# Performance work log

Hardware: AMD Instinct MI355X
Metric: run time of the kernel (lower is better)

## Reference

```python
import jax, jax.numpy as jnp
import numpy as np


def _layernorm(x, g, b, eps=1e-5):
    m = x.mean(-1, keepdims=True)
    v = ((x - m) ** 2).mean(-1, keepdims=True)
    return (x - m) / jnp.sqrt(v + eps) * g + b


def _rotate_every_two(x):
    x1 = x[..., ::2]
    x2 = x[..., 1::2]
    return jnp.stack([-x2, x1], axis=-1).reshape(x.shape)


def _segsum(x):
    # x: (..., L) of negative decay rates -> (..., L, L) bidirectional segment sums
    cs = jnp.cumsum(x, axis=-1)
    d = cs[..., :, None] - cs[..., None, :]
    L = x.shape[-1]
    i = jnp.arange(L)[:, None]
    j = jnp.arange(L)[None, :]
    # lower-tri (incl diag): cs[i]-cs[j]; strict upper: cs[j]-cs[i]; diag is 0
    return jnp.where(i >= j, d, -d)


def _forward(x, y, th, dw1_w, dw1_b, dw2_w, dw2_b, qw, qb, kw, kb, vw, vb,
             lepe_w, lepe_b, dt_w, dt_bias, A_log, ow, ob,
             n1_g, n1_b, ffn_w1, ffn_b1, ffn_w2, ffn_b2, n2_g, n2_b):
    B, C, H, W = x.shape
    nh = dt_bias.shape[0]
    hd = C // nh
    scaling = hd ** (-0.5)

    # dynamic gated fusion of the two kv branches (1x1 convs == channel matmuls)
    fusion = jnp.concatenate([y, th], axis=1)                      # (B,2C,H,W)
    hid = jax.nn.relu(jnp.einsum('bchw,oc->bohw', fusion, dw1_w) + dw1_b[None, :, None, None])
    logits = jnp.einsum('bchw,oc->bohw', hid, dw2_w) + dw2_b[None, :, None, None]
    wts = jax.nn.softmax(logits, axis=1)                           # (B,2,H,W)
    fused = y * wts[:, 0:1] + th * wts[:, 1:2]

    xh = jnp.transpose(x, (0, 2, 3, 1))                            # (B,H,W,C)
    fkv = jnp.transpose(fused, (0, 2, 3, 1))

    # 2D RoPE tables (flattened raster index)
    angle = jnp.repeat(1.0 / 10000 ** jnp.linspace(0.0, 1.0, hd // 2), 2)
    idx = jnp.arange(H * W, dtype=x.dtype)
    sin = jnp.sin(idx[:, None] * angle[None, :]).reshape(H, W, hd)
    cos = jnp.cos(idx[:, None] * angle[None, :]).reshape(H, W, hd)

    q = xh @ qw + qb
    k = fkv @ kw + kb
    v = fkv @ vw + vb

    # depthwise 5x5 conv position term on v (NHWC)
    lepe = jax.lax.conv_general_dilated(
        v, lepe_w, (1, 1), ((2, 2), (2, 2)),
        dimension_numbers=('NHWC', 'HWIO', 'NHWC'), feature_group_count=C) + lepe_b

    k = k * scaling
    q = q.reshape(B, H, W, nh, hd).transpose(0, 3, 1, 2, 4)        # (B,nh,H,W,hd)
    k = k.reshape(B, H, W, nh, hd).transpose(0, 3, 1, 2, 4)
    v5 = v.reshape(B, H, W, nh, hd).transpose(0, 3, 1, 2, 4)

    qr = q * cos + _rotate_every_two(q) * sin
    kr = k * cos + _rotate_every_two(k) * sin

    # PathEmbeding2D: data-dependent decay masks
    xt = xh.reshape(B, H * W, nh, hd)
    dt = xt @ dt_w                                                 # (B,S,nh,2)
    A = -jnp.exp(A_log)                                            # (nh,)
    da = jax.nn.softplus(dt[..., 0] + dt_bias) * A                 # (B,S,nh)
    db = jax.nn.softplus(dt[..., 1] + dt_bias) * A
    mask_w = _segsum(da.reshape(B, H, W, nh).transpose(0, 1, 3, 2))  # (B,H,nh,W,W)
    mask_h = _segsum(db.reshape(B, H, W, nh).transpose(0, 2, 3, 1))  # (B,W,nh,H,H)

    # row (width-direction) and column (height-direction) attentions
    qk_w = jax.nn.softmax(jnp.einsum('bnhid,bnhjd->bhnij', qr, kr) + mask_w, axis=-1)  # (B,H,nh,W,W)
    qk_h = jax.nn.softmax(jnp.einsum('bnhwd,bngwd->bwnhg', qr, kr) + mask_h, axis=-1)  # (B,W,nh,H,H)

    v_w = jnp.einsum('bhnij,bnhjd->bhnid', qk_w, v5)               # (B,H,nh,W,hd)
    out1 = jnp.einsum('bwnhg,bgnwd->bwnhd', qk_h, v_w)             # (B,W,nh,H,hd)
    out1 = out1.transpose(0, 3, 1, 2, 4).reshape(B, H, W, C)

    v_h = jnp.einsum('bwnhg,bngwd->bwnhd', qk_h, v5)               # (B,W,nh,H,hd)
    out2 = jnp.einsum('bhnij,bjnhd->bhnid', qk_w, v_h)             # (B,H,nh,W,hd)
    out2 = out2.transpose(0, 1, 3, 2, 4).reshape(B, H, W, C)

    out = 0.5 * out1 + 0.5 * out2 + lepe
    out = out @ ow + ob
    out = _layernorm(xh + out, n1_g, n1_b)
    ffn = jax.nn.gelu(out @ ffn_w1 + ffn_b1, approximate=False) @ ffn_w2 + ffn_b2
    out = _layernorm(out + ffn, n2_g, n2_b)
    return jnp.transpose(out, (0, 3, 1, 2))                        # (B,C,H,W)


def setup_inputs() -> dict:
    B, C, H, W, nh = 4, 64, 128, 128, 4
    hd = C // nh
    key = jax.random.key(0)
    ks = jax.random.split(key, 20)
    n = lambda k, shp, s: jax.random.normal(k, shp, dtype=jnp.float32) * s
    rng = np.random.default_rng(0)
    dt = np.exp(rng.uniform(0.0, 1.0, nh) * (np.log(0.1) - np.log(0.001)) + np.log(0.001))
    dt = np.clip(dt, 1e-4, None)
    dt_bias = jnp.asarray(dt + np.log(-np.expm1(-dt)), dtype=jnp.float32)
    A_log = jnp.asarray(np.log(rng.uniform(1.0, 1.1, nh)), dtype=jnp.float32)
    inp = {
        'x': n(ks[0], (B, C, H, W), 1.0),
        'y': n(ks[1], (B, C, H, W), 1.0),
        'th': n(ks[2], (B, C, H, W), 1.0),
        'dw1_w': n(ks[3], (C, 2 * C), (2 * C) ** -0.5),
        'dw1_b': jnp.zeros((C,), jnp.float32),
        'dw2_w': n(ks[4], (2, C), C ** -0.5),
        'dw2_b': jnp.zeros((2,), jnp.float32),
        'qw': n(ks[5], (C, C), 0.2 * C ** -0.5),
        'qb': jnp.zeros((C,), jnp.float32),
        'kw': n(ks[6], (C, C), 0.2 * C ** -0.5),
        'kb': jnp.zeros((C,), jnp.float32),
        'vw': n(ks[7], (C, C), 0.2 * C ** -0.5),
        'vb': jnp.zeros((C,), jnp.float32),
        'lepe_w': n(ks[8], (5, 5, 1, C), 0.1),
        'lepe_b': jnp.zeros((C,), jnp.float32),
        'dt_w': n(ks[9], (hd, 2), hd ** -0.5),
        'dt_bias': dt_bias,
        'A_log': A_log,
        'ow': n(ks[10], (C, C), C ** -0.5),
        'ob': jnp.zeros((C,), jnp.float32),
        'n1_g': jnp.ones((C,), jnp.float32),
        'n1_b': jnp.zeros((C,), jnp.float32),
        'ffn_w1': n(ks[11], (C, 4 * C), C ** -0.5),
        'ffn_b1': jnp.zeros((4 * C,), jnp.float32),
        'ffn_w2': n(ks[12], (4 * C, C), (4 * C) ** -0.5),
        'ffn_b2': jnp.zeros((C,), jnp.float32),
        'n2_g': jnp.ones((C,), jnp.float32),
        'n2_b': jnp.zeros((C,), jnp.float32),
    }
    return inp


def reference(x, y, th, dw1_w, dw1_b, dw2_w, dw2_b, qw, qb, kw, kb, vw, vb,
              lepe_w, lepe_b, dt_w, dt_bias, A_log, ow, ob,
              n1_g, n1_b, ffn_w1, ffn_b1, ffn_w2, ffn_b2, n2_g, n2_b):
    return _forward(x, y, th, dw1_w, dw1_b, dw2_w, dw2_b, qw, qb, kw, kb, vw, vb,
                    lepe_w, lepe_b, dt_w, dt_bias, A_log, ow, ob,
                    n1_g, n1_b, ffn_w1, ffn_b1, ffn_w2, ffn_b2, n2_g, n2_b)
```

## Files before the change

### kernel.cpp

```cpp
#include <hip/hip_runtime.h>
#include <math.h>

#define HWSZ 16384

typedef __attribute__((ext_vector_type(8))) short bf16x8;
typedef __attribute__((ext_vector_type(4))) float f32x4;
typedef unsigned short u16;

union U4 { uint4 v; u16 s[8]; };
union U2 { uint2 v; u16 s[4]; };

__device__ __forceinline__ float gelu_f(float v) {
    return 0.5f * v * (1.0f + erff(v * 0.70710678118654752f));
}
__device__ __forceinline__ float splus_f(float v) {
    return (v > 20.f) ? v : log1pf(expf(v));
}
__device__ __forceinline__ u16 f2bf(float f) {
    union { float f; unsigned u; } v; v.f = f;
    unsigned r = (v.u + 0x7FFF + ((v.u >> 16) & 1)) >> 16;
    return (u16)r;
}
__device__ __forceinline__ unsigned pk2(float a, float b) {
    return (unsigned)f2bf(a) | ((unsigned)f2bf(b) << 16);
}
__device__ __forceinline__ float bf2f(u16 s) {
    union { unsigned u; float f; } v; v.u = ((unsigned)s) << 16; return v.f;
}

__global__ __launch_bounds__(256) void k_prep(
    const float* __restrict__ w1, const float* __restrict__ qw,
    const float* __restrict__ kw, const float* __restrict__ vw,
    const float* __restrict__ ow, const float* __restrict__ fw1s,
    const float* __restrict__ fw2s, u16* __restrict__ wout)
{
    int id = blockIdx.x*256 + threadIdx.x;
    float v;
    if (id < 8192) {
        v = w1[id];
    } else if (id < 20480) {
        int t = id - 8192; int m = t >> 12;
        int i = t & 4095; int o = i >> 6, c = i & 63;
        const float* src = (m==0) ? qw : ((m==1) ? kw : vw);
        v = src[c*64 + o];
        if (m == 1) v *= 0.25f;
    } else if (id < 24576) {
        int i = id - 20480; int c = i >> 6, k = i & 63;
        v = ow[k*64 + c];
    } else if (id < 40960) {
        int i = id - 24576; int o = i >> 6, k = i & 63;
        v = fw1s[k*256 + o];
    } else {
        int i = id - 40960; int jc = i >> 12; int r = i & 4095;
        int c = r >> 6, k2 = r & 63;
        v = fw2s[(jc*64 + k2)*64 + c];
    }
    wout[id] = f2bf(v);
}

#define FS 136
__global__ __launch_bounds__(256) void k_fuse(
    const float* __restrict__ y, const float* __restrict__ th,
    const u16* __restrict__ wfuse, const float* __restrict__ b1,
    const float* __restrict__ w2, const float* __restrict__ b2,
    u16* __restrict__ fused)
{
    __shared__ u16 Fsh[128*FS];
    __shared__ u16 Wt[64*FS];
    int tid = threadIdx.x, bid = blockIdx.x;
    int pbase = bid*128;
    int b = pbase >> 14, p0 = pbase & 16383;
    for (int vi = tid; vi < 1024; vi += 256) {
        int cp = vi >> 5;
        int p4 = (vi & 31)*4;
        int c0 = cp*2;
        float4 a = *(const float4*)&y [((size_t)(b*64+c0  ))*HWSZ + p0 + p4];
        float4 c = *(const float4*)&y [((size_t)(b*64+c0+1))*HWSZ + p0 + p4];
        *(unsigned*)&Fsh[(p4+0)*FS + c0] = pk2(a.x, c.x);
        *(unsigned*)&Fsh[(p4+1)*FS + c0] = pk2(a.y, c.y);
        *(unsigned*)&Fsh[(p4+2)*FS + c0] = pk2(a.z, c.z);
        *(unsigned*)&Fsh[(p4+3)*FS + c0] = pk2(a.w, c.w);
        float4 e = *(const float4*)&th[((size_t)(b*64+c0  ))*HWSZ + p0 + p4];
        float4 f = *(const float4*)&th[((size_t)(b*64+c0+1))*HWSZ + p0 + p4];
        *(unsigned*)&Fsh[(p4+0)*FS + 64 + c0] = pk2(e.x, f.x);
        *(unsigned*)&Fsh[(p4+1)*FS + 64 + c0] = pk2(e.y, f.y);
        *(unsigned*)&Fsh[(p4+2)*FS + 64 + c0] = pk2(e.z, f.z);
        *(unsigned*)&Fsh[(p4+3)*FS + 64 + c0] = pk2(e.w, f.w);
    }
    for (int vi = tid; vi < 1024; vi += 256) {
        int o = vi >> 4, s8 = (vi & 15)*8;
        *(uint4*)&Wt[o*FS + s8] = *(const uint4*)&wfuse[o*128 + s8];
    }
    __syncthreads();
    int lane = tid & 63, wv = tid >> 6;
    int quad = lane >> 4, lm = lane & 15;
    int M0 = wv*32;
    f32x4 z = {0.f,0.f,0.f,0.f};
    f32x4 acc[2][4];
    #pragma unroll
    for (int mt = 0; mt < 2; ++mt)
        #pragma unroll
        for (int nt = 0; nt < 4; ++nt) acc[mt][nt] = z;
    #pragma unroll
    for (int ks = 0; ks < 4; ++ks) {
        bf16x8 aF[2];
        #pragma unroll
        for (int mt = 0; mt < 2; ++mt)
            aF[mt] = *(bf16x8*)&Fsh[(M0+mt*16+lm)*FS + ks*32 + quad*8];
        #pragma unroll
        for (int nt = 0; nt < 4; ++nt) {
            bf16x8 bW = *(bf16x8*)&Wt[(nt*16+lm)*FS + ks*32 + quad*8];
            #pragma unroll
            for (int mt = 0; mt < 2; ++mt)
                acc[mt][nt] = __builtin_amdgcn_mfma_f32_16x16x32_bf16(aF[mt], bW, acc[mt][nt], 0,0,0);
        }
    }
    float b1v[4], w2av[4], w2bv[4];
    #pragma unroll
    for (int nt = 0; nt < 4; ++nt) {
        int o = nt*16 + lm;
        b1v[nt] = b1[o]; w2av[nt] = w2[o]; w2bv[nt] = w2[64+o];
    }
    float bias2a = b2[0], bias2b = b2[1];
    size_t gbase = (size_t)(b*16384 + p0);
    #pragma unroll
    for (int mt = 0; mt < 2; ++mt) {
        #pragma unroll
        for (int r = 0; r < 4; ++r) {
            int p = M0 + mt*16 + quad*4 + r;
            float l0 = 0.f, l1 = 0.f;
            #pragma unroll
            for (int nt = 0; nt < 4; ++nt) {
                float h = fmaxf(acc[mt][nt][r] + b1v[nt], 0.f);
                l0 += h * w2av[nt];
                l1 += h * w2bv[nt];
            }
            l0 += __shfl_xor(l0,1,64); l0 += __shfl_xor(l0,2,64);
            l0 += __shfl_xor(l0,4,64); l0 += __shfl_xor(l0,8,64);
            l1 += __shfl_xor(l1,1,64); l1 += __shfl_xor(l1,2,64);
            l1 += __shfl_xor(l1,4,64); l1 += __shfl_xor(l1,8,64);
            l0 += bias2a; l1 += bias2b;
            float m = fmaxf(l0, l1);
            float e0 = __expf(l0 - m), e1 = __expf(l1 - m);
            float inv = 1.f/(e0 + e1);
            float wa = e0*inv, wb = e1*inv;
            U2 yv, tv;
            yv.v = *(uint2*)&Fsh[p*FS + lm*4];
            tv.v = *(uint2*)&Fsh[p*FS + 64 + lm*4];
            unsigned o0 = pk2(bf2f(yv.s[0])*wa + bf2f(tv.s[0])*wb,
                              bf2f(yv.s[1])*wa + bf2f(tv.s[1])*wb);
            unsigned o1 = pk2(bf2f(yv.s[2])*wa + bf2f(tv.s[2])*wb,
                              bf2f(yv.s[3])*wa + bf2f(tv.s[3])*wb);
            *(uint2*)&fused[(gbase + p)*64 + lm*4] = make_uint2(o0, o1);
        }
    }
}

__global__ __launch_bounds__(256) void k_qkv(
    const float* __restrict__ x, const u16* __restrict__ fused,
    const u16* __restrict__ bq, const float* __restrict__ qb,
    const u16* __restrict__ bk, const float* __restrict__ kb,
    const u16* __restrict__ bv, const float* __restrict__ vb,
    const float* __restrict__ dtw, const float* __restrict__ dtb,
    const float* __restrict__ alog,
    u16* __restrict__ qr, u16* __restrict__ kr, u16* __restrict__ v5,
    float* __restrict__ da, float* __restrict__ db)
{
    __shared__ u16 Ax[128*72];
    __shared__ u16 Af[128*72];
    __shared__ u16 Bq[64*72], Bk[64*72], Bv[64*72];
    int tid = threadIdx.x, bid = blockIdx.x;
    int pbase = bid*128;
    int b = pbase >> 14, p0 = pbase & 16383;
    for (int vi = tid; vi < 1024; vi += 256) {
        int cp = vi >> 5, p4 = (vi & 31)*4;
        int c0 = cp*2;
        float4 a = *(const float4*)&x[((size_t)(b*64+c0  ))*HWSZ + p0 + p4];
        float4 c = *(const float4*)&x[((size_t)(b*64+c0+1))*HWSZ + p0 + p4];
        *(unsigned*)&Ax[(p4+0)*72 + c0] = pk2(a.x, c.x);
        *(unsigned*)&Ax[(p4+1)*72 + c0] = pk2(a.y, c.y);
        *(unsigned*)&Ax[(p4+2)*72 + c0] = pk2(a.z, c.z);
        *(unsigned*)&Ax[(p4+3)*72 + c0] = pk2(a.w, c.w);
    }
    for (int vi = tid; vi < 1024; vi += 256) {
        int p = vi >> 3, seg = (vi & 7)*8;
        *(uint4*)&Af[p*72 + seg] = *(const uint4*)&fused[((size_t)(b*16384) + p0 + p)*64 + seg];
    }
    for (int vi = tid; vi < 1536; vi += 256) {
        int m = vi >> 9;
        int i = vi & 511;
        int o = i >> 3, s8 = (i & 7)*8;
        const u16* src = (m==0) ? bq : ((m==1) ? bk : bv);
        u16* dst = (m==0) ? Bq : ((m==1) ? Bk : Bv);
        *(uint4*)&dst[o*72 + s8] = *(const uint4*)&src[o*64 + s8];
    }
    __syncthreads();
    int lane = tid & 63, wv = tid >> 6;
    int quad = lane >> 4, lm = lane & 15;
    int M0 = wv*32;
    f32x4 z = {0.f,0.f,0.f,0.f};
    f32x4 accQ[2][4], accK[2][4], accV[2][4];
    #pragma unroll
    for (int mt = 0; mt < 2; ++mt)
        #pragma unroll
        for (int nt = 0; nt < 4; ++nt) { accQ[mt][nt]=z; accK[mt][nt]=z; accV[mt][nt]=z; }
    #pragma unroll
    for (int ks = 0; ks < 2; ++ks) {
        bf16x8 aX[2], aF[2];
        #pragma unroll
        for (int mt = 0; mt < 2; ++mt) {
            aX[mt] = *(bf16x8*)&Ax[(M0+mt*16+lm)*72 + ks*32 + quad*8];
            aF[mt] = *(bf16x8*)&Af[(M0+mt*16+lm)*72 + ks*32 + quad*8];
        }
        #pragma unroll
        for (int nt = 0; nt < 4; ++nt) {
            bf16x8 bQ = *(bf16x8*)&Bq[(nt*16+lm)*72 + ks*32 + quad*8];
            bf16x8 bK = *(bf16x8*)&Bk[(nt*16+lm)*72 + ks*32 + quad*8];
            bf16x8 bV = *(bf16x8*)&Bv[(nt*16+lm)*72 + ks*32 + quad*8];
            #pragma unroll
            for (int mt = 0; mt < 2; ++mt) {
                accQ[mt][nt] = __builtin_amdgcn_mfma_f32_16x16x32_bf16(aX[mt], bQ, accQ[mt][nt], 0,0,0);
                accK[mt][nt] = __builtin_amdgcn_mfma_f32_16x16x32_bf16(aF[mt], bK, accK[mt][nt], 0,0,0);
                accV[mt][nt] = __builtin_amdgcn_mfma_f32_16x16x32_bf16(aF[mt], bV, accV[mt][nt], 0,0,0);
            }
        }
    }
    {
        float dtw_[32];
        #pragma unroll
        for (int i = 0; i < 32; ++i) dtw_[i] = dtw[i];
        #pragma unroll
        for (int rep = 0; rep < 2; ++rep) {
            int pair = tid + rep*256;
            int p = pair >> 2, n = pair & 3;
            float dt0 = 0.f, dt1 = 0.f;
            #pragma unroll
            for (int d = 0; d < 16; ++d) {
                float xv = bf2f(Ax[p*72 + n*16 + d]);
                dt0 += xv*dtw_[2*d];
                dt1 += xv*dtw_[2*d+1];
            }
            float A = -expf(alog[n]);
            float bb = dtb[n];
            int P = p0 + p;
            int h = P >> 7, w = P & 127;
            da[((b*128+h)*4+n)*128 + w] = splus_f(dt0+bb)*A;
            db[((b*128+w)*4+n)*128 + h] = splus_f(dt1+bb)*A;
        }
    }
    float qbv[4], kbv[4], vbv[4];
    #pragma unroll
    for (int nt = 0; nt < 4; ++nt) {
        qbv[nt] = qb[nt*16+lm]; kbv[nt] = kb[nt*16+lm]*0.25f; vbv[nt] = vb[nt*16+lm];
    }
    bool evn = !(lm & 1);
    float ang = exp2f(-1.89824462565f * (float)(lm >> 1));
    int bb4 = b*4;
    #pragma unroll
    for (int mt = 0; mt < 2; ++mt) {
        #pragma unroll
        for (int r = 0; r < 4; ++r) {
            int P = p0 + M0 + mt*16 + quad*4 + r;
            float sn_, cs_;
            sincosf((float)P * ang, &sn_, &cs_);
            #pragma unroll
            for (int nt = 0; nt < 4; ++nt) {
                float vq = accQ[mt][nt][r] + qbv[nt];
                float pq = __shfl_xor(vq, 1, 64);
                float rq = evn ? vq*cs_ - pq*sn_ : vq*cs_ + pq*sn_;
                unsigned uq = f2bf(rq);
                unsigned upq = (unsigned)__shfl_xor((int)uq, 1, 64);
                float vk = accK[mt][nt][r] + kbv[nt];
                float pk = __shfl_xor(vk, 1, 64);
                float rk = evn ? vk*cs_ - pk*sn_ : vk*cs_ + pk*sn_;
                unsigned uk = f2bf(rk);
                unsigned upk = (unsigned)__shfl_xor((int)uk, 1, 64);
                unsigned uv = f2bf(accV[mt][nt][r] + vbv[nt]);
                unsigned upv = (unsigned)__shfl_xor((int)uv, 1, 64);
                if (evn) {
                    size_t off = ((size_t)(bb4+nt)*HWSZ + P)*16 + lm;
                    *(unsigned*)&qr[off] = (uq & 0xffff) | (upq << 16);
                    *(unsigned*)&kr[off] = (uk & 0xffff) | (upk << 16);
                    *(unsigned*)&v5[off] = (uv & 0xffff) | (upv << 16);
                }
            }
        }
    }
}

#define LROW 328
__global__ __launch_bounds__(256) void k_lepe(
    const u16* __restrict__ v5, const float* __restrict__ lw,
    const float* __restrict__ lb, u16* __restrict__ lepe)
{
    __shared__ float sv[36*LROW];
    __shared__ float swt[400];
    int tid = threadIdx.x, bid = blockIdx.x;
    int tw = bid & 7, th_ = (bid >> 3) & 3, n = (bid >> 5) & 3, b = bid >> 7;
    int bn = b*4 + n;
    int h0 = th_*32, w0 = tw*16;
    for (int i = tid; i < 400; i += 256) {
        int tap = i >> 4, d = i & 15;
        swt[i] = lw[tap*64 + n*16 + d];
    }
    const u16* vb = v5 + (size_t)bn*HWSZ*16;
    for (int vi = tid; vi < 1440; vi += 256) {
        int cell = vi >> 1, half = vi & 1;
        int hh = cell/20, ww = cell - hh*20;
        int h = h0 - 2 + hh, w = w0 - 2 + ww;
        U4 val; val.v = make_uint4(0,0,0,0);
        if (h >= 0 && h < 128 && w >= 0 && w < 128)
            val.v = *(const uint4*)&vb[((size_t)(h*128+w))*16 + half*8];
        float* dst = &sv[hh*LROW + ww*16 + half*8];
        #pragma unroll
        for (int u = 0; u < 8; ++u) dst[u] = bf2f(val.s[u]);
    }
    __syncthreads();
    int df = (tid & 3)*4;
    int s  = tid >> 2;
    int ph = s >> 1;
    int pw = (s & 1)*8;
    float4 bv = *(const float4*)&lb[n*16 + df];
    float acc[8][4];
    #pragma unroll
    for (int ow = 0; ow < 8; ++ow) {
        acc[ow][0] = bv.x; acc[ow][1] = bv.y; acc[ow][2] = bv.z; acc[ow][3] = bv.w;
    }
    #pragma unroll
    for (int ky = 0; ky < 5; ++ky) {
        float wgt[5][4];
        #pragma unroll
        for (int kx = 0; kx < 5; ++kx) {
            float4 wv = *(const float4*)&swt[(ky*5+kx)*16 + df];
            wgt[kx][0]=wv.x; wgt[kx][1]=wv.y; wgt[kx][2]=wv.z; wgt[kx][3]=wv.w;
        }
        float dat[13][4];
        #pragma unroll
        for (int c = 0; c < 13; ++c) {
            float4 dv = *(const float4*)&sv[(ph+ky)*LROW + (pw+c)*16 + df];
            dat[c][0]=dv.x; dat[c][1]=dv.y; dat[c][2]=dv.z; dat[c][3]=dv.w;
        }
        #pragma unroll
        for (int ow = 0; ow < 8; ++ow)
            #pragma unroll
            for (int kx = 0; kx < 5; ++kx)
                #pragma unroll
                for (int u = 0; u < 4; ++u)
                    acc[ow][u] += dat[ow+kx][u]*wgt[kx][u];
    }
    u16* ob = lepe + ((size_t)bn*HWSZ + (size_t)(h0+ph)*128 + w0+pw)*16 + df;
    #pragma unroll
    for (int ow = 0; ow < 8; ++ow)
        *(uint2*)&ob[ow*16] = make_uint2(pk2(acc[ow][0],acc[ow][1]), pk2(acc[ow][2],acc[ow][3]));
}

__global__ __launch_bounds__(256) void k_attn_w1(
    const u16* __restrict__ qr, const u16* __restrict__ kr,
    const u16* __restrict__ v5, const float* __restrict__ dacs,
    u16* __restrict__ vwb)
{
    __shared__ u16 Vt[16*136], Ps[128*136];
    __shared__ float csr[128];
    int tid = threadIdx.x, bid = blockIdx.x;
    int h = bid & 127, n = (bid >> 7) & 3, b = bid >> 9;
    size_t rowoff = ((size_t)((b*4+n)*128 + h)) * 2048;
    {
        int jp = tid >> 2, q4 = tid & 3;
        U2 a, c;
        a.v = *(const uint2*)&v5[rowoff + (2*jp)*16 + q4*4];
        c.v = *(const uint2*)&v5[rowoff + (2*jp+1)*16 + q4*4];
        #pragma unroll
        for (int u = 0; u < 4; ++u)
            *(unsigned*)&Vt[(q4*4+u)*136 + 2*jp] = (unsigned)a.s[u] | ((unsigned)c.s[u] << 16);
    }
    if (tid < 128) csr[tid] = dacs[((b*128+h)*4+n)*128 + tid];
    __syncthreads();
    if (tid < 64) {
        float2 e = *(float2*)&csr[tid*2];
        float s = e.x + e.y;
        #pragma unroll
        for (int d = 1; d < 64; d <<= 1) {
            float t = __shfl_up(s, d, 64);
            if (tid >= d) s += t;
        }
        csr[tid*2]   = s - e.y;
        csr[tid*2+1] = s;
    }
    __syncthreads();
    int lane = tid & 63, wv = tid >> 6;
    int quad = lane >> 4, lm = lane & 15;
    int r0 = wv*32, r1 = wv*32 + 16;
    bf16x8 z8 = {0,0,0,0,0,0,0,0};
    bf16x8 aQ0 = z8, aQ1 = z8;
    if (quad < 2) {
        aQ0 = *(const bf16x8*)&qr[rowoff + (size_t)(r0+lm)*16 + quad*8];
        aQ1 = *(const bf16x8*)&qr[rowoff + (size_t)(r1+lm)*16 + quad*8];
    }
    float csj[8], csi0[4], csi1[4];
    #pragma unroll
    for (int jt = 0; jt < 8; ++jt) csj[jt] = csr[jt*16+lm];
    #pragma unroll
    for (int r = 0; r < 4; ++r) { csi0[r] = csr[r0+quad*4+r]; csi1[r] = csr[r1+quad*4+r]; }
    float ls0[4]={0,0,0,0}, ls1[4]={0,0,0,0};
    f32x4 z = {0.f,0.f,0.f,0.f};
    #pragma unroll
    for (int jt = 0; jt < 8; ++jt) {
        bf16x8 bK = z8;
        if (quad < 2) bK = *(const bf16x8*)&kr[rowoff + (size_t)(jt*16+lm)*16 + quad*8];
        f32x4 s0 = __builtin_amdgcn_mfma_f32_16x16x32_bf16(aQ0, bK, z, 0,0,0);
        f32x4 s1 = __builtin_amdgcn_mfma_f32_16x16x32_bf16(aQ1, bK, z, 0,0,0);
        #pragma unroll
        for (int r = 0; r < 4; ++r) {
            float e0 = __expf(s0[r] - fabsf(csi0[r]-csj[jt])); ls0[r] += e0;
            float e1 = __expf(s1[r] - fabsf(csi1[r]-csj[jt])); ls1[r] += e1;
            Ps[(r0+quad*4+r)*136 + jt*16+lm] = f2bf(e0);
            Ps[(r1+quad*4+r)*136 + jt*16+lm] = f2bf(e1);
        }
    }
    float inv0[4], inv1[4];
    #pragma unroll
    for (int r = 0; r < 4; ++r) {
        #pragma unroll
        for (int m = 1; m < 16; m <<= 1) {
            ls0[r] += __shfl_xor(ls0[r], m, 64);
            ls1[r] += __shfl_xor(ls1[r], m, 64);
        }
        inv0[r] = 1.f/ls0[r]; inv1[r] = 1.f/ls1[r];
    }
    __syncthreads();
    f32x4 acc0 = z, acc1 = z;
    #pragma unroll
    for (int c = 0; c < 4; ++c) {
        bf16x8 bV  = *(bf16x8*)&Vt[lm*136 + c*32 + quad*8];
        bf16x8 aP0 = *(bf16x8*)&Ps[(r0+lm)*136 + c*32 + quad*8];
        bf16x8 aP1 = *(bf16x8*)&Ps[(r1+lm)*136 + c*32 + quad*8];
        acc0 = __builtin_amdgcn_mfma_f32_16x16x32_bf16(aP0, bV, acc0, 0,0,0);
        acc1 = __builtin_amdgcn_mfma_f32_16x16x32_bf16(aP1, bV, acc1, 0,0,0);
    }
    bool evn = !(lm & 1);
    #pragma unroll
    for (int r = 0; r < 4; ++r) {
        int i0 = r0+quad*4+r, i1 = r1+quad*4+r;
        unsigned u0 = f2bf(acc0[r]*inv0[r]);
        unsigned u1 = f2bf(acc1[r]*inv1[r]);
        unsigned up0 = (unsigned)__shfl_xor((int)u0, 1, 64);
        unsigned up1 = (unsigned)__shfl_xor((int)u1, 1, 64);
        if (evn) {
            *(unsigned*)&vwb[rowoff + (size_t)i0*16 + lm] = (u0 & 0xffff) | (up0 << 16);
            *(unsigned*)&vwb[rowoff + (size_t)i1*16 + lm] = (u1 & 0xffff) | (up1 << 16);
        }
    }
}

__global__ __launch_bounds__(256) void k_attn_h(
    const u16* __restrict__ qr, const u16* __restrict__ kr,
    const u16* __restrict__ v5, const u16* __restrict__ vwb,
    const float* __restrict__ dbcs,
    u16* __restrict__ vhb, u16* __restrict__ o1b)
{
    __shared__ u16 Vt[16*136], Wt[16*136], Ps[128*136];
    __shared__ float csr[128];
    int tid = threadIdx.x, bid = blockIdx.x;
    int w = bid & 127, n = (bid >> 7) & 3, b = bid >> 9;
    int bn = b*4 + n;
    size_t base = ((size_t)bn*16384 + w)*16;
    {
        int jp = tid >> 2, q4 = tid & 3;
        U2 a, c, e, f;
        a.v = *(const uint2*)&v5 [base + (size_t)(2*jp)*2048 + q4*4];
        c.v = *(const uint2*)&v5 [base + (size_t)(2*jp+1)*2048 + q4*4];
        e.v = *(const uint2*)&vwb[base + (size_t)(2*jp)*2048 + q4*4];
        f.v = *(const uint2*)&vwb[base + (size_t)(2*jp+1)*2048 + q4*4];
        #pragma unroll
        for (int u = 0; u < 4; ++u) {
            *(unsigned*)&Vt[(q4*4+u)*136 + 2*jp] = (unsigned)a.s[u] | ((unsigned)c.s[u] << 16);
            *(unsigned*)&Wt[(q4*4+u)*136 + 2*jp] = (unsigned)e.s[u] | ((unsigned)f.s[u] << 16);
        }
    }
    if (tid < 128) csr[tid] = dbcs[((b*128+w)*4+n)*128 + tid];
    __syncthreads();
    if (tid < 64) {
        float2 e = *(float2*)&csr[tid*2];
        float s = e.x + e.y;
        #pragma unroll
        for (int d = 1; d < 64; d <<= 1) {
            float t = __shfl_up(s, d, 64);
            if (tid >= d) s += t;
        }
        csr[tid*2]   = s - e.y;
        csr[tid*2+1] = s;
    }
    __syncthreads();
    int lane = tid & 63, wv = tid >> 6;
    int quad = lane >> 4, lm = lane & 15;
    int r0 = wv*32, r1 = wv*32 + 16;
    bf16x8 z8 = {0,0,0,0,0,0,0,0};
    bf16x8 aQ0 = z8, aQ1 = z8;
    if (quad < 2) {
        aQ0 = *(const bf16x8*)&qr[base + (size_t)(r0+lm)*2048 + quad*8];
        aQ1 = *(const bf16x8*)&qr[base + (size_t)(r1+lm)*2048 + quad*8];
    }
    float csj[8], csi0[4], csi1[4];
    #pragma unroll
    for (int jt = 0; jt < 8; ++jt) csj[jt] = csr[jt*16+lm];
    #pragma unroll
    for (int r = 0; r < 4; ++r) { csi0[r] = csr[r0+quad*4+r]; csi1[r] = csr[r1+quad*4+r]; }
    float ls0[4]={0,0,0,0}, ls1[4]={0,0,0,0};
    f32x4 z = {0.f,0.f,0.f,0.f};
    #pragma unroll
    for (int jt = 0; jt < 8; ++jt) {
        bf16x8 bK = z8;
        if (quad < 2) bK = *(const bf16x8*)&kr[base + (size_t)(jt*16+lm)*2048 + quad*8];
        f32x4 s0 = __builtin_amdgcn_mfma_f32_16x16x32_bf16(aQ0, bK, z, 0,0,0);
        f32x4 s1 = __builtin_amdgcn_mfma_f32_16x16x32_bf16(aQ1, bK, z, 0,0,0);
        #pragma unroll
        for (int r = 0; r < 4; ++r) {
            float e0 = __expf(s0[r] - fabsf(csi0[r]-csj[jt])); ls0[r] += e0;
            float e1 = __expf(s1[r] - fabsf(csi1[r]-csj[jt])); ls1[r] += e1;
            Ps[(r0+quad*4+r)*136 + jt*16+lm] = f2bf(e0);
            Ps[(r1+quad*4+r)*136 + jt*16+lm] = f2bf(e1);
        }
    }
    float inv0[4], inv1[4];
    #pragma unroll
    for (int r = 0; r < 4; ++r) {
        #pragma unroll
        for (int m = 1; m < 16; m <<= 1) {
            ls0[r] += __shfl_xor(ls0[r], m, 64);
            ls1[r] += __shfl_xor(ls1[r], m, 64);
        }
        inv0[r] = 1.f/ls0[r]; inv1[r] = 1.f/ls1[r];
    }
    __syncthreads();
    f32x4 aV0 = z, aV1 = z, aW0 = z, aW1 = z;
    #pragma unroll
    for (int c = 0; c < 4; ++c) {
        bf16x8 bV  = *(bf16x8*)&Vt[lm*136 + c*32 + quad*8];
        bf16x8 bW  = *(bf16x8*)&Wt[lm*136 + c*32 + quad*8];
        bf16x8 aP0 = *(bf16x8*)&Ps[(r0+lm)*136 + c*32 + quad*8];
        bf16x8 aP1 = *(bf16x8*)&Ps[(r1+lm)*136 + c*32 + quad*8];
        aV0 = __builtin_amdgcn_mfma_f32_16x16x32_bf16(aP0, bV, aV0, 0,0,0);
        aV1 = __builtin_amdgcn_mfma_f32_16x16x32_bf16(aP1, bV, aV1, 0,0,0);
        aW0 = __builtin_amdgcn_mfma_f32_16x16x32_bf16(aP0, bW, aW0, 0,0,0);
        aW1 = __builtin_amdgcn_mfma_f32_16x16x32_bf16(aP1, bW, aW1, 0,0,0);
    }
    size_t obase = ((size_t)bn*16384 + (size_t)w*128)*16;
    bool evn = !(lm & 1);
    #pragma unroll
    for (int r = 0; r < 4; ++r) {
        int i0 = r0+quad*4+r, i1 = r1+quad*4+r;
        float v0 = inv0[r], v1 = inv1[r];
        unsigned a0 = f2bf(aV0[r]*v0), a1 = f2bf(aV1[r]*v1);
        unsigned b0 = f2bf(aW0[r]*v0), b1 = f2bf(aW1[r]*v1);
        unsigned ap0 = (unsigned)__shfl_xor((int)a0,1,64), ap1 = (unsigned)__shfl_xor((int)a1,1,64);
        unsigned bp0 = (unsigned)__shfl_xor((int)b0,1,64), bp1 = (unsigned)__shfl_xor((int)b1,1,64);
        if (evn) {
            *(unsigned*)&vhb[obase + (size_t)i0*16 + lm] = (a0 & 0xffff) | (ap0 << 16);
            *(unsigned*)&vhb[obase + (size_t)i1*16 + lm] = (a1 & 0xffff) | (ap1 << 16);
            *(unsigned*)&o1b[obase + (size_t)i0*16 + lm] = (b0 & 0xffff) | (bp0 << 16);
            *(unsigned*)&o1b[obase + (size_t)i1*16 + lm] = (b1 & 0xffff) | (bp1 << 16);
        }
    }
}

__global__ __launch_bounds__(256) void k_attn_w2(
    const u16* __restrict__ qr, const u16* __restrict__ kr,
    const u16* __restrict__ vhb, const u16* __restrict__ o1b,
    const float* __restrict__ dacs, const u16* __restrict__ lepe,
    u16* __restrict__ attn)
{
    __shared__ u16 Vt[16*136], Ps[128*136];
    __shared__ float csr[128];
    int tid = threadIdx.x, bid = blockIdx.x;
    int h = bid & 127, n = (bid >> 7) & 3, b = bid >> 9;
    int bn = b*4 + n;
    size_t rowoff = ((size_t)(bn*128 + h)) * 2048;
    size_t vbase  = (size_t)bn*262144 + (size_t)h*16;
    {
        int jp = tid >> 2, q4 = tid & 3;
        U2 a, c;
        a.v = *(const uint2*)&vhb[vbase + (size_t)(2*jp)*2048 + q4*4];
        c.v = *(const uint2*)&vhb[vbase + (size_t)(2*jp+1)*2048 + q4*4];
        #pragma unroll
        for (int u = 0; u < 4; ++u)
            *(unsigned*)&Vt[(q4*4+u)*136 + 2*jp] = (unsigned)a.s[u] | ((unsigned)c.s[u] << 16);
    }
    if (tid < 128) csr[tid] = dacs[((b*128+h)*4+n)*128 + tid];
    __syncthreads();
    if (tid < 64) {
        float2 e = *(float2*)&csr[tid*2];
        float s = e.x + e.y;
        #pragma unroll
        for (int d = 1; d < 64; d <<= 1) {
            float t = __shfl_up(s, d, 64);
            if (tid >= d) s += t;
        }
        csr[tid*2]   = s - e.y;
        csr[tid*2+1] = s;
    }
    __syncthreads();
    int lane = tid & 63, wv = tid >> 6;
    int quad = lane >> 4, lm = lane & 15;
    int r0 = wv*32, r1 = wv*32 + 16;
    bf16x8 z8 = {0,0,0,0,0,0,0,0};
    bf16x8 aQ0 = z8, aQ1 = z8;
    if (quad < 2) {
        aQ0 = *(const bf16x8*)&qr[rowoff + (size_t)(r0+lm)*16 + quad*8];
        aQ1 = *(const bf16x8*)&qr[rowoff + (size_t)(r1+lm)*16 + quad*8];
    }
    float csj[8], csi0[4], csi1[4];
    #pragma unroll
    for (int jt = 0; jt < 8; ++jt) csj[jt] = csr[jt*16+lm];
    #pragma unroll
    for (int r = 0; r < 4; ++r) { csi0[r] = csr[r0+quad*4+r]; csi1[r] = csr[r1+quad*4+r]; }
    float ls0[4]={0,0,0,0}, ls1[4]={0,0,0,0};
    f32x4 z = {0.f,0.f,0.f,0.f};
    #pragma unroll
    for (int jt = 0; jt < 8; ++jt) {
        bf16x8 bK = z8;
        if (quad < 2) bK = *(const bf16x8*)&kr[rowoff + (size_t)(jt*16+lm)*16 + quad*8];
        f32x4 s0 = __builtin_amdgcn_mfma_f32_16x16x32_bf16(aQ0, bK, z, 0,0,0);
        f32x4 s1 = __builtin_amdgcn_mfma_f32_16x16x32_bf16(aQ1, bK, z, 0,0,0);
        #pragma unroll
        for (int r = 0; r < 4; ++r) {
            float e0 = __expf(s0[r] - fabsf(csi0[r]-csj[jt])); ls0[r] += e0;
            float e1 = __expf(s1[r] - fabsf(csi1[r]-csj[jt])); ls1[r] += e1;
            Ps[(r0+quad*4+r)*136 + jt*16+lm] = f2bf(e0);
            Ps[(r1+quad*4+r)*136 + jt*16+lm] = f2bf(e1);
        }
    }
    float inv0[4], inv1[4];
    #pragma unroll
    for (int r = 0; r < 4; ++r) {
        #pragma unroll
        for (int m = 1; m < 16; m <<= 1) {
            ls0[r] += __shfl_xor(ls0[r], m, 64);
            ls1[r] += __shfl_xor(ls1[r], m, 64);
        }
        inv0[r] = 1.f/ls0[r]; inv1[r] = 1.f/ls1[r];
    }
    __syncthreads();
    f32x4 acc0 = z, acc1 = z;
    #pragma unroll
    for (int c = 0; c < 4; ++c) {
        bf16x8 bV  = *(bf16x8*)&Vt[lm*136 + c*32 + quad*8];
        bf16x8 aP0 = *(bf16x8*)&Ps[(r0+lm)*136 + c*32 + quad*8];
        bf16x8 aP1 = *(bf16x8*)&Ps[(r1+lm)*136 + c*32 + quad*8];
        acc0 = __builtin_amdgcn_mfma_f32_16x16x32_bf16(aP0, bV, acc0, 0,0,0);
        acc1 = __builtin_amdgcn_mfma_f32_16x16x32_bf16(aP1, bV, acc1, 0,0,0);
    }
    size_t lpb = (size_t)bn*262144 + (size_t)h*2048;
    size_t oab = (size_t)b*1048576 + (size_t)h*8192 + n*16;
    bool evn = !(lm & 1);
    #pragma unroll
    for (int r = 0; r < 4; ++r) {
        int i0 = r0+quad*4+r, i1 = r1+quad*4+r;
        float o2a = acc0[r]*inv0[r];
        float o2b = acc1[r]*inv1[r];
        float o1a = bf2f(o1b[vbase + (size_t)i0*2048 + lm]);
        float o1c = bf2f(o1b[vbase + (size_t)i1*2048 + lm]);
        float la  = bf2f(lepe[lpb + (size_t)i0*16 + lm]);
        float lc  = bf2f(lepe[lpb + (size_t)i1*16 + lm]);
        unsigned ua = f2bf(0.5f*(o1a + o2a) + la);
        unsigned uc = f2bf(0.5f*(o1c + o2b) + lc);
        unsigned upa = (unsigned)__shfl_xor((int)ua,1,64);
        unsigned upc = (unsigned)__shfl_xor((int)uc,1,64);
        if (evn) {
            *(unsigned*)&attn[oab + (size_t)i0*64 + lm] = (ua & 0xffff) | (upa << 16);
            *(unsigned*)&attn[oab + (size_t)i1*64 + lm] = (uc & 0xffff) | (upc << 16);
        }
    }
}

__global__ __launch_bounds__(256) void k_proj_ln(
    const u16* __restrict__ attn, const float* __restrict__ x,
    const u16* __restrict__ bo, const float* __restrict__ ob,
    const float* __restrict__ g1, const float* __restrict__ b1,
    u16* __restrict__ t1)
{
    __shared__ u16 As[64*72];
    __shared__ u16 Bs[64*72];
    __shared__ float XT[64*68];
    int tid = threadIdx.x, bid = blockIdx.x;
    int pbase = bid*64;
    int b = pbase >> 14, p0 = pbase & 16383;
    for (int vi = tid; vi < 512; vi += 256) {
        int p = vi >> 3, s8 = (vi & 7)*8;
        *(uint4*)&As[p*72 + s8] = *(const uint4*)&attn[((size_t)(pbase+p))*64 + s8];
    }
    for (int vi = tid; vi < 512; vi += 256) {
        int c = vi >> 3, s8 = (vi & 7)*8;
        *(uint4*)&Bs[c*72 + s8] = *(const uint4*)&bo[c*64 + s8];
    }
    for (int vi = tid; vi < 1024; vi += 256) {
        int c = vi >> 4, p4 = (vi & 15)*4;
        *(float4*)&XT[c*68 + p4] = *(const float4*)&x[((size_t)(b*64+c))*HWSZ + p0 + p4];
    }
    __syncthreads();
    int lane = tid & 63, wv = tid >> 6;
    int quad = lane >> 4, lm = lane & 15;
    int M0 = wv*16;
    float xv[4][4], obv[4], g1v[4], b1v[4];
    #pragma unroll
    for (int nt = 0; nt < 4; ++nt) {
        int c = nt*16 + lm;
        obv[nt] = ob[c]; g1v[nt] = g1[c]; b1v[nt] = b1[c];
        #pragma unroll
        for (int r = 0; r < 4; ++r)
            xv[nt][r] = XT[c*68 + M0 + quad*4 + r];
    }
    f32x4 z = {0.f,0.f,0.f,0.f};
    f32x4 acc[4];
    #pragma unroll
    for (int nt = 0; nt < 4; ++nt) acc[nt] = z;
    #pragma unroll
    for (int ks = 0; ks < 2; ++ks) {
        bf16x8 aF = *(bf16x8*)&As[(M0+lm)*72 + ks*32 + quad*8];
        #pragma unroll
        for (int nt = 0; nt < 4; ++nt) {
            bf16x8 bF = *(bf16x8*)&Bs[(nt*16+lm)*72 + ks*32 + quad*8];
            acc[nt] = __builtin_amdgcn_mfma_f32_16x16x32_bf16(aF, bF, acc[nt], 0,0,0);
        }
    }
    float val[4][4], res[4][4];
    #pragma unroll
    for (int r = 0; r < 4; ++r) {
        float s = 0.f;
        #pragma unroll
        for (int nt = 0; nt < 4; ++nt) {
            val[nt][r] = acc[nt][r] + obv[nt] + xv[nt][r];
            s += val[nt][r];
        }
        s += __shfl_xor(s, 1, 64); s += __shfl_xor(s, 2, 64);
        s += __shfl_xor(s, 4, 64); s += __shfl_xor(s, 8, 64);
        float mean = s*(1.f/64.f);
        float vv = 0.f;
        #pragma unroll
        for (int nt = 0; nt < 4; ++nt) {
            float d = val[nt][r] - mean;
            vv += d*d;
        }
// ... 107 lines not shown
        #pragma unroll
        for (int nt = 0; nt < 4; ++nt) {
            float tv = bf2f(At1[pos*72 + nt*16 + lm]);
            val[nt][r] = acc2[nt][r] + sb2v[nt] + tv;
            s += val[nt][r];
        }
        s += __shfl_xor(s, 1, 64); s += __shfl_xor(s, 2, 64);
        s += __shfl_xor(s, 4, 64); s += __shfl_xor(s, 8, 64);
        float mean = s*(1.f/64.f);
        float vv = 0.f;
        #pragma unroll
        for (int nt = 0; nt < 4; ++nt) {
            float d = val[nt][r] - mean;
            vv += d*d;
        }
        vv += __shfl_xor(vv, 1, 64); vv += __shfl_xor(vv, 2, 64);
        vv += __shfl_xor(vv, 4, 64); vv += __shfl_xor(vv, 8, 64);
        float rs = rsqrtf(vv*(1.f/64.f) + 1e-5f);
        #pragma unroll
        for (int nt = 0; nt < 4; ++nt)
            res[nt][r] = (val[nt][r] - mean)*rs*sgv[nt] + sbbv[nt];
    }
    __syncthreads();
    float* outT = (float*)SL;
    #pragma unroll
    for (int r = 0; r < 4; ++r)
        #pragma unroll
        for (int nt = 0; nt < 4; ++nt)
            outT[(nt*16+lm)*68 + M0 + quad*4 + r] = res[nt][r];
    __syncthreads();
    for (int vi = tid; vi < 1024; vi += 256) {
        int c = vi >> 4, p4 = (vi & 15)*4;
        *(float4*)&outp[((size_t)(b*64+c))*HWSZ + p0 + p4] = *(const float4*)&outT[c*68 + p4];
    }
}

extern "C" void kernel_launch(void* const* d_in, const int* in_sizes, int n_in,
                              void* d_out, int out_size, void* d_ws, size_t ws_size,
                              hipStream_t stream) {
    const float* x      = (const float*)d_in[0];
    const float* y      = (const float*)d_in[1];
    const float* th     = (const float*)d_in[2];
    const float* dw1_w  = (const float*)d_in[3];
    const float* dw1_b  = (const float*)d_in[4];
    const float* dw2_w  = (const float*)d_in[5];
    const float* dw2_b  = (const float*)d_in[6];
    const float* qw     = (const float*)d_in[7];
    const float* qb     = (const float*)d_in[8];
    const float* kw     = (const float*)d_in[9];
    const float* kb     = (const float*)d_in[10];
    const float* vw     = (const float*)d_in[11];
    const float* vb     = (const float*)d_in[12];
    const float* lepe_w = (const float*)d_in[13];
    const float* lepe_b = (const float*)d_in[14];
    const float* dt_w   = (const float*)d_in[15];
    const float* dt_bias= (const float*)d_in[16];
    const float* A_log  = (const float*)d_in[17];
    const float* ow     = (const float*)d_in[18];
    const float* ob     = (const float*)d_in[19];
    const float* n1_g   = (const float*)d_in[20];
    const float* n1_b   = (const float*)d_in[21];
    const float* ffn_w1 = (const float*)d_in[22];
    const float* ffn_b1 = (const float*)d_in[23];
    const float* ffn_w2 = (const float*)d_in[24];
    const float* ffn_b2 = (const float*)d_in[25];
    const float* n2_g   = (const float*)d_in[26];
    const float* n2_b   = (const float*)d_in[27];
    float* out = (float*)d_out;

    const size_t SZ = 4194304;
    float* ws    = (float*)d_ws;
    u16* fused = (u16*)(ws + 0*SZ);
    u16* qrb   = (u16*)(ws + 1*SZ);
    u16* krb   = (u16*)(ws + 2*SZ);
    u16* v5b   = (u16*)(ws + 3*SZ);
    u16* lepeb = (u16*)(ws + 4*SZ);
    u16* vhb   = (u16*)(ws + 5*SZ);
    u16* o1b   = (u16*)(ws + 6*SZ);
    u16* attnb = (u16*)(ws + 7*SZ);
    u16* t1b   = (u16*)(ws + 8*SZ);
    float* dacs  = ws + 9*SZ;
    float* dbcs  = ws + 9*SZ + 262144;
    u16* wall  = (u16*)(ws + 9*SZ + 524288);
    u16* wfuse = wall;
    u16* bq    = wall + 8192;
    u16* bk    = wall + 12288;
    u16* bv    = wall + 16384;
    u16* bo    = wall + 20480;
    u16* fw1   = wall + 24576;
    u16* fw2   = wall + 40960;

    k_prep<<<224, 256, 0, stream>>>(dw1_w, qw, kw, vw, ow, ffn_w1, ffn_w2, wall);
    k_fuse<<<512, 256, 0, stream>>>(y, th, wfuse, dw1_b, dw2_w, dw2_b, fused);
    k_qkv<<<512, 256, 0, stream>>>(x, fused, bq, qb, bk, kb, bv, vb,
                                   dt_w, dt_bias, A_log, qrb, krb, v5b, dacs, dbcs);
    k_lepe<<<512, 256, 0, stream>>>(v5b, lepe_w, lepe_b, lepeb);
    k_attn_w1<<<2048, 256, 0, stream>>>(qrb, krb, v5b, dacs, fused);
    k_attn_h<<<2048, 256, 0, stream>>>(qrb, krb, v5b, fused, dbcs, vhb, o1b);
    k_attn_w2<<<2048, 256, 0, stream>>>(qrb, krb, vhb, o1b, dacs, lepeb, attnb);
    k_proj_ln<<<1024, 256, 0, stream>>>(attnb, x, bo, ob, n1_g, n1_b, t1b);
    k_ffn<<<1024, 256, 0, stream>>>(t1b, fw1, ffn_b1, fw2, ffn_b2, n2_g, n2_b, out);
}
```

Measured before the change: 292.6 us.

## Compute softmax denominators via MFMA, precompute RoPE table, vectorize dt loads

The three attention kernels no longer sum exponentials in scalar code and reduce them with 4-step shuffles. They now get the row sums from an extra MFMA against a vector of bf16 ones, which sums the bf16-rounded probabilities. RoPE sin/cos values are computed once per position in the prep kernel into a table, replacing the per-element sincosf in k_qkv. The dt projection also loads its LDS inputs as vectors. Costs are extra MFMA work, a global table read, and a larger prep grid.

```diff
diff --git a/kernel.cpp b/kernel.cpp
--- a/kernel.cpp
+++ b/kernel.cpp
@@ -32,30 +32,40 @@
     const float* __restrict__ w1, const float* __restrict__ qw,
     const float* __restrict__ kw, const float* __restrict__ vw,
     const float* __restrict__ ow, const float* __restrict__ fw1s,
-    const float* __restrict__ fw2s, u16* __restrict__ wout)
+    const float* __restrict__ fw2s, u16* __restrict__ wout,
+    float* __restrict__ rope)
 {
     int id = blockIdx.x*256 + threadIdx.x;
-    float v;
-    if (id < 8192) {
-        v = w1[id];
-    } else if (id < 20480) {
-        int t = id - 8192; int m = t >> 12;
-        int i = t & 4095; int o = i >> 6, c = i & 63;
-        const float* src = (m==0) ? qw : ((m==1) ? kw : vw);
-        v = src[c*64 + o];
-        if (m == 1) v *= 0.25f;
-    } else if (id < 24576) {
-        int i = id - 20480; int c = i >> 6, k = i & 63;
-        v = ow[k*64 + c];
-    } else if (id < 40960) {
-        int i = id - 24576; int o = i >> 6, k = i & 63;
-        v = fw1s[k*256 + o];
+    if (id < 57344) {
+        float v;
+        if (id < 8192) {
+            v = w1[id];
+        } else if (id < 20480) {
+            int t = id - 8192; int m = t >> 12;
+            int i = t & 4095; int o = i >> 6, c = i & 63;
+            const float* src = (m==0) ? qw : ((m==1) ? kw : vw);
+            v = src[c*64 + o];
+            if (m == 1) v *= 0.25f;
+        } else if (id < 24576) {
+            int i = id - 20480; int c = i >> 6, k = i & 63;
+            v = ow[k*64 + c];
+        } else if (id < 40960) {
+            int i = id - 24576; int o = i >> 6, k = i & 63;
+            v = fw1s[k*256 + o];
+        } else {
+            int i = id - 40960; int jc = i >> 12; int r = i & 4095;
+            int c = r >> 6, k2 = r & 63;
+            v = fw2s[(jc*64 + k2)*64 + c];
+        }
+        wout[id] = f2bf(v);
     } else {
-        int i = id - 40960; int jc = i >> 12; int r = i & 4095;
-        int c = r >> 6, k2 = r & 63;
-        v = fw2s[(jc*64 + k2)*64 + c];
-    }
-    wout[id] = f2bf(v);
+        int idx = id - 57344;
+        int P = idx >> 4, j = idx & 15;
+        int pr = j >> 1;
+        float ang = exp2f(-1.89824462565f * (float)pr);
+        float v = (float)P * ang;
+        rope[idx] = (j & 1) ? cosf(v) : sinf(v);
+    }
 }
 
 #define FS 136
@@ -162,7 +172,7 @@
     const u16* __restrict__ bk, const float* __restrict__ kb,
     const u16* __restrict__ bv, const float* __restrict__ vb,
     const float* __restrict__ dtw, const float* __restrict__ dtb,
-    const float* __restrict__ alog,
+    const float* __restrict__ alog, const float* __restrict__ rope,
     u16* __restrict__ qr, u16* __restrict__ kr, u16* __restrict__ v5,
     float* __restrict__ da, float* __restrict__ db)
 {
@@ -233,12 +243,21 @@
         for (int rep = 0; rep < 2; ++rep) {
             int pair = tid + rep*256;
             int p = pair >> 2, n = pair & 3;
+            U4 a, c;
+            a.v = *(const uint4*)&Ax[p*72 + n*16];
+            c.v = *(const uint4*)&Ax[p*72 + n*16 + 8];
             float dt0 = 0.f, dt1 = 0.f;
             #pragma unroll
-            for (int d = 0; d < 16; ++d) {
-                float xv = bf2f(Ax[p*72 + n*16 + d]);
+            for (int d = 0; d < 8; ++d) {
+                float xv = bf2f(a.s[d]);
                 dt0 += xv*dtw_[2*d];
                 dt1 += xv*dtw_[2*d+1];
+            }
+            #pragma unroll
+            for (int d = 0; d < 8; ++d) {
+                float xv = bf2f(c.s[d]);
+                dt0 += xv*dtw_[16+2*d];
+                dt1 += xv*dtw_[16+2*d+1];
             }
             float A = -expf(alog[n]);
             float bb = dtb[n];
@@ -254,15 +273,14 @@
         qbv[nt] = qb[nt*16+lm]; kbv[nt] = kb[nt*16+lm]*0.25f; vbv[nt] = vb[nt*16+lm];
     }
     bool evn = !(lm & 1);
-    float ang = exp2f(-1.89824462565f * (float)(lm >> 1));
     int bb4 = b*4;
     #pragma unroll
     for (int mt = 0; mt < 2; ++mt) {
         #pragma unroll
         for (int r = 0; r < 4; ++r) {
             int P = p0 + M0 + mt*16 + quad*4 + r;
-            float sn_, cs_;
-            sincosf((float)P * ang, &sn_, &cs_);
+            float2 sc = *(const float2*)&rope[(size_t)P*16 + (lm >> 1)*2];
+            float sn_ = sc.x, cs_ = sc.y;
             #pragma unroll
             for (int nt = 0; nt < 4; ++nt) {
                 float vq = accQ[mt][nt][r] + qbv[nt];
@@ -391,6 +409,9 @@
     int quad = lane >> 4, lm = lane & 15;
     int r0 = wv*32, r1 = wv*32 + 16;
     bf16x8 z8 = {0,0,0,0,0,0,0,0};
+    bf16x8 one8;
+    #pragma unroll
+    for (int i = 0; i < 8; ++i) one8[i] = (short)0x3F80;
     bf16x8 aQ0 = z8, aQ1 = z8;
     if (quad < 2) {
         aQ0 = *(const bf16x8*)&qr[rowoff + (size_t)(r0+lm)*16 + quad*8];
@@ -401,7 +422,6 @@
     for (int jt = 0; jt < 8; ++jt) csj[jt] = csr[jt*16+lm];
     #pragma unroll
     for (int r = 0; r < 4; ++r) { csi0[r] = csr[r0+quad*4+r]; csi1[r] = csr[r1+quad*4+r]; }
-    float ls0[4]={0,0,0,0}, ls1[4]={0,0,0,0};
     f32x4 z = {0.f,0.f,0.f,0.f};
     #pragma unroll
     for (int jt = 0; jt < 8; ++jt) {
@@ -411,24 +431,14 @@
         f32x4 s1 = __builtin_amdgcn_mfma_f32_16x16x32_bf16(aQ1, bK, z, 0,0,0);
         #pragma unroll
         for (int r = 0; r < 4; ++r) {
-            float e0 = __expf(s0[r] - fabsf(csi0[r]-csj[jt])); ls0[r] += e0;
-            float e1 = __expf(s1[r] - fabsf(csi1[r]-csj[jt])); ls1[r] += e1;
+            float e0 = __expf(s0[r] - fabsf(csi0[r]-csj[jt]));
+            float e1 = __expf(s1[r] - fabsf(csi1[r]-csj[jt]));
             Ps[(r0+quad*4+r)*136 + jt*16+lm] = f2bf(e0);
             Ps[(r1+quad*4+r)*136 + jt*16+lm] = f2bf(e1);
         }
     }
-    float inv0[4], inv1[4];
-    #pragma unroll
-    for (int r = 0; r < 4; ++r) {
-        #pragma unroll
-        for (int m = 1; m < 16; m <<= 1) {
-            ls0[r] += __shfl_xor(ls0[r], m, 64);
-            ls1[r] += __shfl_xor(ls1[r], m, 64);
-        }
-        inv0[r] = 1.f/ls0[r]; inv1[r] = 1.f/ls1[r];
-    }
-    __syncthreads();
-    f32x4 acc0 = z, acc1 = z;
+    __syncthreads();
+    f32x4 acc0 = z, acc1 = z, den0 = z, den1 = z;
     #pragma unroll
     for (int c = 0; c < 4; ++c) {
         bf16x8 bV  = *(bf16x8*)&Vt[lm*136 + c*32 + quad*8];
@@ -436,13 +446,15 @@
         bf16x8 aP1 = *(bf16x8*)&Ps[(r1+lm)*136 + c*32 + quad*8];
         acc0 = __builtin_amdgcn_mfma_f32_16x16x32_bf16(aP0, bV, acc0, 0,0,0);
         acc1 = __builtin_amdgcn_mfma_f32_16x16x32_bf16(aP1, bV, acc1, 0,0,0);
+        den0 = __builtin_amdgcn_mfma_f32_16x16x32_bf16(aP0, one8, den0, 0,0,0);
+        den1 = __builtin_amdgcn_mfma_f32_16x16x32_bf16(aP1, one8, den1, 0,0,0);
     }
     bool evn = !(lm & 1);
     #pragma unroll
     for (int r = 0; r < 4; ++r) {
         int i0 = r0+quad*4+r, i1 = r1+quad*4+r;
-        unsigned u0 = f2bf(acc0[r]*inv0[r]);
-        unsigned u1 = f2bf(acc1[r]*inv1[r]);
+        unsigned u0 = f2bf(acc0[r]/den0[r]);
+        unsigned u1 = f2bf(acc1[r]/den1[r]);
         unsigned up0 = (unsigned)__shfl_xor((int)u0, 1, 64);
         unsigned up1 = (unsigned)__shfl_xor((int)u1, 1, 64);
         if (evn) {
@@ -495,6 +507,9 @@
     int quad = lane >> 4, lm = lane & 15;
     int r0 = wv*32, r1 = wv*32 + 16;
     bf16x8 z8 = {0,0,0,0,0,0,0,0};
+    bf16x8 one8;
+    #pragma unroll
+    for (int i = 0; i < 8; ++i) one8[i] = (short)0x3F80;
     bf16x8 aQ0 = z8, aQ1 = z8;
     if (quad < 2) {
         aQ0 = *(const bf16x8*)&qr[base + (size_t)(r0+lm)*2048 + quad*8];
@@ -505,7 +520,6 @@
     for (int jt = 0; jt < 8; ++jt) csj[jt] = csr[jt*16+lm];
     #pragma unroll
     for (int r = 0; r < 4; ++r) { csi0[r] = csr[r0+quad*4+r]; csi1[r] = csr[r1+quad*4+r]; }
-    float ls0[4]={0,0,0,0}, ls1[4]={0,0,0,0};
     f32x4 z = {0.f,0.f,0.f,0.f};
     #pragma unroll
     for (int jt = 0; jt < 8; ++jt) {
@@ -515,24 +529,14 @@
         f32x4 s1 = __builtin_amdgcn_mfma_f32_16x16x32_bf16(aQ1, bK, z, 0,0,0);
         #pragma unroll
         for (int r = 0; r < 4; ++r) {
-            float e0 = __expf(s0[r] - fabsf(csi0[r]-csj[jt])); ls0[r] += e0;
-            float e1 = __expf(s1[r] - fabsf(csi1[r]-csj[jt])); ls1[r] += e1;
+            float e0 = __expf(s0[r] - fabsf(csi0[r]-csj[jt]));
+            float e1 = __expf(s1[r] - fabsf(csi1[r]-csj[jt]));
             Ps[(r0+quad*4+r)*136 + jt*16+lm] = f2bf(e0);
             Ps[(r1+quad*4+r)*136 + jt*16+lm] = f2bf(e1);
         }
     }
-    float inv0[4], inv1[4];
-    #pragma unroll
-    for (int r = 0; r < 4; ++r) {
-        #pragma unroll
-        for (int m = 1; m < 16; m <<= 1) {
-            ls0[r] += __shfl_xor(ls0[r], m, 64);
-            ls1[r] += __shfl_xor(ls1[r], m, 64);
-        }
-        inv0[r] = 1.f/ls0[r]; inv1[r] = 1.f/ls1[r];
-    }
-    __syncthreads();
-    f32x4 aV0 = z, aV1 = z, aW0 = z, aW1 = z;
+    __syncthreads();
+    f32x4 aV0 = z, aV1 = z, aW0 = z, aW1 = z, den0 = z, den1 = z;
     #pragma unroll
     for (int c = 0; c < 4; ++c) {
         bf16x8 bV  = *(bf16x8*)&Vt[lm*136 + c*32 + quad*8];
@@ -543,13 +547,15 @@
         aV1 = __builtin_amdgcn_mfma_f32_16x16x32_bf16(aP1, bV, aV1, 0,0,0);
         aW0 = __builtin_amdgcn_mfma_f32_16x16x32_bf16(aP0, bW, aW0, 0,0,0);
         aW1 = __builtin_amdgcn_mfma_f32_16x16x32_bf16(aP1, bW, aW1, 0,0,0);
+        den0 = __builtin_amdgcn_mfma_f32_16x16x32_bf16(aP0, one8, den0, 0,0,0);
+        den1 = __builtin_amdgcn_mfma_f32_16x16x32_bf16(aP1, one8, den1, 0,0,0);
     }
     size_t obase = ((size_t)bn*16384 + (size_t)w*128)*16;
     bool evn = !(lm & 1);
     #pragma unroll
     for (int r = 0; r < 4; ++r) {
         int i0 = r0+quad*4+r, i1 = r1+quad*4+r;
-        float v0 = inv0[r], v1 = inv1[r];
+        float v0 = 1.f/den0[r], v1 = 1.f/den1[r];
         unsigned a0 = f2bf(aV0[r]*v0), a1 = f2bf(aV1[r]*v1);
         unsigned b0 = f2bf(aW0[r]*v0), b1 = f2bf(aW1[r]*v1);
         unsigned ap0 = (unsigned)__shfl_xor((int)a0,1,64), ap1 = (unsigned)__shfl_xor((int)a1,1,64);
@@ -603,6 +609,9 @@
     int quad = lane >> 4, lm = lane & 15;
     int r0 = wv*32, r1 = wv*32 + 16;
     bf16x8 z8 = {0,0,0,0,0,0,0,0};
+    bf16x8 one8;
+    #pragma unroll
+    for (int i = 0; i < 8; ++i) one8[i] = (short)0x3F80;
     bf16x8 aQ0 = z8, aQ1 = z8;
     if (quad < 2) {
         aQ0 = *(const bf16x8*)&qr[rowoff + (size_t)(r0+lm)*16 + quad*8];
@@ -613,7 +622,6 @@
     for (int jt = 0; jt < 8; ++jt) csj[jt] = csr[jt*16+lm];
     #pragma unroll
     for (int r = 0; r < 4; ++r) { csi0[r] = csr[r0+quad*4+r]; csi1[r] = csr[r1+quad*4+r]; }
-    float ls0[4]={0,0,0,0}, ls1[4]={0,0,0,0};
     f32x4 z = {0.f,0.f,0.f,0.f};
     #pragma unroll
     for (int jt = 0; jt < 8; ++jt) {
@@ -623,24 +631,14 @@
         f32x4 s1 = __builtin_amdgcn_mfma_f32_16x16x32_bf16(aQ1, bK, z, 0,0,0);
         #pragma unroll
         for (int r = 0; r < 4; ++r) {
-            float e0 = __expf(s0[r] - fabsf(csi0[r]-csj[jt])); ls0[r] += e0;
-            float e1 = __expf(s1[r] - fabsf(csi1[r]-csj[jt])); ls1[r] += e1;
+            float e0 = __expf(s0[r] - fabsf(csi0[r]-csj[jt]));
+            float e1 = __expf(s1[r] - fabsf(csi1[r]-csj[jt]));
             Ps[(r0+quad*4+r)*136 + jt*16+lm] = f2bf(e0);
             Ps[(r1+quad*4+r)*136 + jt*16+lm] = f2bf(e1);
         }
     }
-    float inv0[4], inv1[4];
-    #pragma unroll
-    for (int r = 0; r < 4; ++r) {
-        #pragma unroll
-        for (int m = 1; m < 16; m <<= 1) {
-            ls0[r] += __shfl_xor(ls0[r], m, 64);
-            ls1[r] += __shfl_xor(ls1[r], m, 64);
-        }
-        inv0[r] = 1.f/ls0[r]; inv1[r] = 1.f/ls1[r];
-    }
-    __syncthreads();
-    f32x4 acc0 = z, acc1 = z;
+    __syncthreads();
+    f32x4 acc0 = z, acc1 = z, den0 = z, den1 = z;
     #pragma unroll
     for (int c = 0; c < 4; ++c) {
         bf16x8 bV  = *(bf16x8*)&Vt[lm*136 + c*32 + quad*8];
@@ -648,6 +646,8 @@
         bf16x8 aP1 = *(bf16x8*)&Ps[(r1+lm)*136 + c*32 + quad*8];
         acc0 = __builtin_amdgcn_mfma_f32_16x16x32_bf16(aP0, bV, acc0, 0,0,0);
         acc1 = __builtin_amdgcn_mfma_f32_16x16x32_bf16(aP1, bV, acc1, 0,0,0);
+        den0 = __builtin_amdgcn_mfma_f32_16x16x32_bf16(aP0, one8, den0, 0,0,0);
+        den1 = __builtin_amdgcn_mfma_f32_16x16x32_bf16(aP1, one8, den1, 0,0,0);
     }
     size_t lpb = (size_t)bn*262144 + (size_t)h*2048;
     size_t oab = (size_t)b*1048576 + (size_t)h*8192 + n*16;
@@ -655,8 +655,8 @@
     #pragma unroll
     for (int r = 0; r < 4; ++r) {
         int i0 = r0+quad*4+r, i1 = r1+quad*4+r;
-        float o2a = acc0[r]*inv0[r];
-        float o2b = acc1[r]*inv1[r];
+        float o2a = acc0[r]/den0[r];
+        float o2b = acc1[r]/den1[r];
         float o1a = bf2f(o1b[vbase + (size_t)i0*2048 + lm]);
         float o1c = bf2f(o1b[vbase + (size_t)i1*2048 + lm]);
         float la  = bf2f(lepe[lpb + (size_t)i0*16 + lm]);
@@ -930,6 +930,7 @@
     float* dacs  = ws + 9*SZ;
     float* dbcs  = ws + 9*SZ + 262144;
     u16* wall  = (u16*)(ws + 9*SZ + 524288);
+    float* rope  = ws + 9*SZ + 524288 + 28672;
     u16* wfuse = wall;
     u16* bq    = wall + 8192;
     u16* bk    = wall + 12288;
@@ -938,10 +939,10 @@
     u16* fw1   = wall + 24576;
     u16* fw2   = wall + 40960;
 
-    k_prep<<<224, 256, 0, stream>>>(dw1_w, qw, kw, vw, ow, ffn_w1, ffn_w2, wall);
+    k_prep<<<1248, 256, 0, stream>>>(dw1_w, qw, kw, vw, ow, ffn_w1, ffn_w2, wall, rope);
     k_fuse<<<512, 256, 0, stream>>>(y, th, wfuse, dw1_b, dw2_w, dw2_b, fused);
     k_qkv<<<512, 256, 0, stream>>>(x, fused, bq, qb, bk, kb, bv, vb,
-                                   dt_w, dt_bias, A_log, qrb, krb, v5b, dacs, dbcs);
+                                   dt_w, dt_bias, A_log, rope, qrb, krb, v5b, dacs, dbcs);
     k_lepe<<<512, 256, 0, stream>>>(v5b, lepe_w, lepe_b, lepeb);
     k_attn_w1<<<2048, 256, 0, stream>>>(qrb, krb, v5b, dacs, fused);
     k_attn_h<<<2048, 256, 0, stream>>>(qrb, krb, v5b, fused, dbcs, vhb, o1b);
```

Result: slower. 305.3 us (+4.3%).
